# Kernel optimization log

Hardware: AMD Instinct MI355X
Metric: run time of the kernel (lower is better)

The kernel has to match this reference:

```python
import jax, jax.numpy as jnp
import numpy as np

N = 100_000      # nodes
E = 1_600_000    # edges (avg degree 16)
F_IN = 32        # node_feat_dim
HID = 32         # hidden_dim
OUT = 1          # out_dim


def setup_inputs() -> dict:
    key = jax.random.key(0)
    ks = jax.random.split(key, 16)
    x = jax.random.normal(ks[0], (N, F_IN), dtype=jnp.float32)
    # edge_index with no self loops (PyG ChebConv removes them anyway)
    src = jax.random.randint(ks[1], (E,), 0, N, dtype=jnp.int32)
    off = jax.random.randint(ks[2], (E,), 1, N, dtype=jnp.int32)
    dst = ((src + off) % N).astype(jnp.int32)
    edge_index = jnp.stack([src, dst])

    def glorot(k, shape, fan_in, fan_out):
        s = (2.0 / (fan_in + fan_out)) ** 0.5
        return (s * jax.random.normal(k, shape)).astype(jnp.float32)

    inp = {"x": x, "edge_index": edge_index}
    names = ["xz", "hz", "xr", "hr", "xh", "hh"]
    for i, nm in enumerate(names):
        fan = F_IN if nm[0] == "x" else HID
        inp[f"W_{nm}"] = glorot(ks[3 + i], (2, fan, HID), fan, HID)  # ChebConv K=2
        inp[f"b_{nm}"] = jnp.zeros((HID,), jnp.float32)
    inp["W_gcn"] = glorot(ks[9], (HID, HID), HID, HID)
    inp["b_gcn"] = jnp.zeros((HID,), jnp.float32)
    inp["W_lin"] = glorot(ks[10], (HID, OUT), HID, OUT)
    inp["b_lin"] = jnp.zeros((OUT,), jnp.float32)
    return inp


def _forward(x, edge_index, W_xz, b_xz, W_hz, b_hz, W_xr, b_xr, W_hr, b_hr,
             W_xh, b_xh, W_hh, b_hh, W_gcn, b_gcn, W_lin, b_lin):
    src, dst = edge_index[0], edge_index[1]
    ones = jnp.ones((src.shape[0],), x.dtype)

    def agg(w, v):  # out[i] = sum_{e: dst_e = i} w_e * v[src_e]
        return jax.ops.segment_sum(w[:, None] * v[src], dst, num_segments=N)

    # --- ChebConv (sym norm, lambda_max=2): L_hat = -D^{-1/2} A D^{-1/2} ---
    deg = jax.ops.segment_sum(ones, src, num_segments=N)
    dis = jnp.where(deg > 0, jax.lax.rsqrt(jnp.maximum(deg, 1.0)), 0.0)
    lap_w = -(dis[src] * dis[dst])

    def cheb(v, W, b):  # K=2: x @ W0 + (L_hat x) @ W1 + b
        return v @ W[0] + agg(lap_w, v) @ W[1] + b

    # --- GConvGRU single step, H0 = 0 ---
    H0 = jnp.zeros((N, HID), x.dtype)
    Z = jax.nn.sigmoid(cheb(x, W_xz, b_xz) + cheb(H0, W_hz, b_hz))
    R = jax.nn.sigmoid(cheb(x, W_xr, b_xr) + cheb(H0, W_hr, b_hr))
    Ht = jnp.tanh(cheb(x, W_xh, b_xh) + cheb(H0 * R, W_hh, b_hh))
    H = Z * H0 + (1.0 - Z) * Ht

    # --- GCNConv with added self loops (deg includes self loop) ---
    deg_g = jax.ops.segment_sum(ones, dst, num_segments=N) + 1.0
    disg = jax.lax.rsqrt(deg_g)
    gw = disg[src] * disg[dst]
    hw = H @ W_gcn
    h = agg(gw, hw) + (disg * disg)[:, None] * hw + b_gcn  # neighbors + self loop
    h = jax.nn.relu(h)

    out = h @ W_lin + b_lin
    return out.squeeze(-1)


def reference(x, edge_index, W_xz, b_xz, W_hz, b_hz, W_xr, b_xr, W_hr, b_hr,
              W_xh, b_xh, W_hh, b_hh, W_gcn, b_gcn, W_lin, b_lin):
    return _forward(x, edge_index, W_xz, b_xz, W_hz, b_hz, W_xr, b_xr, W_hr, b_hr,
                    W_xh, b_xh, W_hh, b_hh, W_gcn, b_gcn, W_lin, b_lin)
```

## Files before the change

kernel.cpp:

```cpp
#include <hip/hip_runtime.h>
#include <hip/hip_fp16.h>

#define NN 100000
#define NE 1600000
#define NB 391
#define NBLK 391
#define CHUNK 4096
#define BT 1024
#define PT 1024
#define ASTR 8192

__device__ __forceinline__ float h16lo(unsigned u) {
    return __half2float(__ushort_as_half((unsigned short)(u & 0xffffu)));
}
__device__ __forceinline__ float h16hi(unsigned u) {
    return __half2float(__ushort_as_half((unsigned short)(u >> 16)));
}
__device__ __forceinline__ unsigned short h16(float f) {
    return __half_as_ushort(__float2half(f));
}
__device__ __forceinline__ unsigned pack2h(float a, float b) {
    return (unsigned)h16(a) | ((unsigned)h16(b) << 16);
}

using f16x8  = __attribute__((ext_vector_type(8)))  _Float16;
using f32x16 = __attribute__((ext_vector_type(16))) float;

__global__ __launch_bounds__(BT) void k_bucket(
        const int* __restrict__ src, const int* __restrict__ dst,
        int* __restrict__ cur_d, int* __restrict__ cur_s,
        unsigned* __restrict__ bkd, unsigned char* __restrict__ bks) {
    __shared__ int hd[NB], hs[NB];
    __shared__ int bd[NB], bs[NB];
    __shared__ int od[NB], os[NB];
    __shared__ int t0[512], t1[512];
    __shared__ unsigned       sortd[CHUNK];
    __shared__ unsigned short sbkt [CHUNK];
    __shared__ unsigned char  sorts[CHUNK];
    __shared__ unsigned short sbkts[CHUNK];

    int tid = threadIdx.x, blk = blockIdx.x;
    if (tid < NB) { hd[tid] = 0; hs[tid] = 0; }
    __syncthreads();

    int e0 = blk * CHUNK, ee = min(e0 + CHUNK, NE);
    int sv[4], dv[4]; bool va[4];
#pragma unroll
    for (int u = 0; u < 4; ++u) {
        int e = e0 + u * BT + tid;
        va[u] = e < ee;
        if (va[u]) {
            sv[u] = src[e]; dv[u] = dst[e];
            atomicAdd(&hd[dv[u] >> 8], 1);
            atomicAdd(&hs[sv[u] >> 8], 1);
        }
    }
    __syncthreads();

    if (tid < 512) {
        t0[tid] = tid < NB ? hd[tid] : 0;
        t1[tid] = tid < NB ? hs[tid] : 0;
    }
    __syncthreads();
    for (int off = 1; off < 512; off <<= 1) {
        int a = 0, b = 0;
        if (tid < 512 && tid >= off) { a = t0[tid - off]; b = t1[tid - off]; }
        __syncthreads();
        if (tid < 512) { t0[tid] += a; t1[tid] += b; }
        __syncthreads();
    }
    if (tid < NB) {
        int c = hd[tid], c2 = hs[tid];
        od[tid] = t0[tid] - c;
        os[tid] = t1[tid] - c2;
        bd[tid] = c  ? atomicAdd(&cur_d[tid], c)  : 0;
        bs[tid] = c2 ? atomicAdd(&cur_s[tid], c2) : 0;
        hd[tid] = od[tid];
        hs[tid] = os[tid];
    }
    __syncthreads();

#pragma unroll
    for (int u = 0; u < 4; ++u) if (va[u]) {
        int bu = dv[u] >> 8;
        int p = atomicAdd(&hd[bu], 1);
        sortd[p] = ((unsigned)(dv[u] & 255) << 17) | (unsigned)sv[u];
        sbkt[p]  = (unsigned short)bu;
        int bv = sv[u] >> 8;
        int q = atomicAdd(&hs[bv], 1);
        sorts[q] = (unsigned char)(sv[u] & 255);
        sbkts[q] = (unsigned short)bv;
    }
    __syncthreads();

    int n = ee - e0;
    for (int i = tid; i < n; i += BT) {
        int b1 = sbkt[i];
        bkd[b1 * ASTR + bd[b1] + (i - od[b1])] = sortd[i];
        int b2 = sbkts[i];
        bks[b2 * ASTR + bs[b2] + (i - os[b2])] = sorts[i];
    }
}

__global__ __launch_bounds__(PT) void k_p2(const unsigned* __restrict__ bkd,
                                           const unsigned char* __restrict__ bks,
                                           const int* __restrict__ cur_d,
                                           const int* __restrict__ cur_s,
                                           int* __restrict__ cd,
                                           int* __restrict__ start,
                                           int* __restrict__ csr_s,
                                           float* __restrict__ dis,
                                           float* __restrict__ disg) {
    __shared__ int hist[256], scn[256], hsA[256];
    __shared__ int red[PT];
    int b = blockIdx.x, tid = threadIdx.x;
    if (tid < 256) { hist[tid] = 0; hsA[tid] = 0; }
    int acc = 0;
    for (int i = tid; i < b; i += PT) acc += cur_d[i];
    red[tid] = acc;
    __syncthreads();
    for (int off = PT / 2; off > 0; off >>= 1) {
        if (tid < off) red[tid] += red[tid + off];
        __syncthreads();
    }
    int cb = red[0];

    int eb = b * ASTR, ee = eb + cur_d[b];
    for (int e = eb + tid; e < ee; e += PT)
        atomicAdd(&hist[bkd[e] >> 17], 1);
    int sb = b * ASTR, se = sb + cur_s[b];
    for (int e = sb + tid; e < se; e += PT)
        atomicAdd(&hsA[bks[e]], 1);
    __syncthreads();
    int c = (tid < 256) ? hist[tid] : 0;
    if (tid < 256) scn[tid] = c;
    __syncthreads();
    for (int off = 1; off < 256; off <<= 1) {
        int t = (tid < 256 && tid >= off) ? scn[tid - off] : 0;
        __syncthreads();
        if (tid < 256) scn[tid] += t;
        __syncthreads();
    }
    if (tid < 256) {
        int excl = scn[tid] - c;
        int node = (b << 8) + tid;
        if (node < NN) {
            cd[node] = c;
            start[node] = cb + excl;
            int oc = hsA[tid];
            dis[node]  = oc > 0 ? rsqrtf((float)oc) : 0.0f;
            disg[node] = rsqrtf((float)c + 1.0f);
        }
    }
    __syncthreads();
    if (tid < 256) hsA[tid] = cb + scn[tid] - c;
    __syncthreads();
    for (int e = eb + tid; e < ee; e += PT) {
        unsigned pk = bkd[e];
        int p = atomicAdd(&hsA[pk >> 17], 1);
        csr_s[p] = (int)(pk & 0x1FFFFu);
    }
}

__global__ __launch_bounds__(256) void k_cvt(const float* __restrict__ x,
                                             const float* __restrict__ dis,
                                             unsigned short* __restrict__ xs,
                                             const float* __restrict__ W_xz,
                                             const float* __restrict__ W_xh,
                                             const float* __restrict__ W_gcn,
                                             unsigned short* __restrict__ BzT,
                                             unsigned short* __restrict__ BhT,
                                             unsigned short* __restrict__ WgT) {
    int tid = threadIdx.x;
    int i = blockIdx.x * 256 + tid;
    if (i < NN * 32) {
        xs[i] = h16(x[i] * dis[i >> 5]);
    } else if (blockIdx.x == (NN * 32) / 256) {
        for (int idx = tid; idx < 2048; idx += 256) {
            int f = idx >> 6, k = idx & 63;
            float vz = (k < 32) ? W_xz[k * 32 + f] : W_xz[1024 + (k - 32) * 32 + f];
            float vh = (k < 32) ? W_xh[k * 32 + f] : W_xh[1024 + (k - 32) * 32 + f];
            BzT[idx] = h16(vz);
            BhT[idx] = h16(vh);
        }
        for (int idx = tid; idx < 1024; idx += 256) {
            int f = idx >> 5, k = idx & 31;
            WgT[idx] = h16(W_gcn[k * 32 + f]);
        }
    }
}

__global__ __launch_bounds__(256) void k_gath_lx(const uint2* __restrict__ xs2,
                                                 const int* __restrict__ csr_s,
                                                 const int* __restrict__ start,
                                                 const int* __restrict__ cd,
                                                 const float* __restrict__ dis,
                                                 unsigned* __restrict__ Lxh) {
    int tid = threadIdx.x;
    int node = blockIdx.x * 8 + (tid >> 5);
    int lane = tid & 31, eoff = lane >> 3, c = lane & 7;
    int st = start[node], cn = cd[node];

    float a0 = 0.f, a1 = 0.f, a2 = 0.f, a3 = 0.f;
    for (int j = 0; j < cn; j += 8) {
        int e0 = j + eoff, e1 = j + 4 + eoff;
        int c0 = e0 < cn ? e0 : cn - 1;  float m0 = e0 < cn ? 1.0f : 0.0f;
        int c1 = e1 < cn ? e1 : cn - 1;  float m1 = e1 < cn ? 1.0f : 0.0f;
        int s0 = csr_s[st + c0], s1 = csr_s[st + c1];
        uint2 v0 = xs2[s0 * 8 + c];
        uint2 v1 = xs2[s1 * 8 + c];
        a0 = fmaf(m0, h16lo(v0.x), a0);  a1 = fmaf(m0, h16hi(v0.x), a1);
        a2 = fmaf(m0, h16lo(v0.y), a2);  a3 = fmaf(m0, h16hi(v0.y), a3);
        a0 = fmaf(m1, h16lo(v1.x), a0);  a1 = fmaf(m1, h16hi(v1.x), a1);
        a2 = fmaf(m1, h16lo(v1.y), a2);  a3 = fmaf(m1, h16hi(v1.y), a3);
    }
#pragma unroll
    for (int off = 8; off < 32; off <<= 1) {
        a0 += __shfl_xor(a0, off, 32);  a1 += __shfl_xor(a1, off, 32);
        a2 += __shfl_xor(a2, off, 32);  a3 += __shfl_xor(a3, off, 32);
    }
    if (lane < 8) {
        float w = -dis[node];
        Lxh[node * 16 + 2 * lane]     = pack2h(w * a0, w * a1);
        Lxh[node * 16 + 2 * lane + 1] = pack2h(w * a2, w * a3);
    }
}

__global__ __launch_bounds__(256) void k_dmm(
        const float* __restrict__ x,
        const f16x8* __restrict__ Lxh,
        const f16x8* __restrict__ BzT,
        const f16x8* __restrict__ BhT,
        const f16x8* __restrict__ WgT,
        const float* __restrict__ b_xz, const float* __restrict__ b_hz,
        const float* __restrict__ b_xh, const float* __restrict__ b_hh,
        const float* __restrict__ disg,
        unsigned short* __restrict__ hws) {
    __shared__ unsigned short Hl[4 * 1280];
    int tid = threadIdx.x;
    int wv = blockIdx.x * 4 + (tid >> 6);
    if (wv > 3124) wv = 3124;
    int l = tid & 63, mrow = l & 31, hi = l >> 5;
    int n0 = wv * 32;
    unsigned short* Hw = Hl + (tid >> 6) * 1280;

    f32x16 accz = {}, acct = {};
    const float* xrow = x + (size_t)(n0 + mrow) * 32;
#pragma unroll
    for (int c = 0; c < 2; ++c) {
        f16x8 a;
        const float* p = xrow + c * 16 + hi * 8;
#pragma unroll
        for (int e = 0; e < 8; ++e) a[e] = (_Float16)p[e];
        accz = __builtin_amdgcn_mfma_f32_32x32x16_f16(a, BzT[mrow * 8 + c * 2 + hi], accz, 0, 0, 0);
        acct = __builtin_amdgcn_mfma_f32_32x32x16_f16(a, BhT[mrow * 8 + c * 2 + hi], acct, 0, 0, 0);
    }
    const f16x8* Lrow = Lxh + (size_t)(n0 + mrow) * 4;
#pragma unroll
    for (int c = 2; c < 4; ++c) {
        f16x8 a = Lrow[(c - 2) * 2 + hi];
        accz = __builtin_amdgcn_mfma_f32_32x32x16_f16(a, BzT[mrow * 8 + c * 2 + hi], accz, 0, 0, 0);
        acct = __builtin_amdgcn_mfma_f32_32x32x16_f16(a, BhT[mrow * 8 + c * 2 + hi], acct, 0, 0, 0);
    }
    float bz = b_xz[mrow] + b_hz[mrow];
    float bh = b_xh[mrow] + b_hh[mrow];
#pragma unroll
    for (int j = 0; j < 16; ++j) {
        float z = accz[j] + bz, t = acct[j] + bh;
        float Z = 1.0f / (1.0f + expf(-z));
        float H = (1.0f - Z) * tanhf(t);
        int r = (j & 3) + 8 * (j >> 2) + 4 * hi;
        Hw[r * 40 + mrow] = h16(H);
    }
    f32x16 acch = {};
#pragma unroll
    for (int c = 0; c < 2; ++c) {
        f16x8 hfrag = *reinterpret_cast<const f16x8*>(&Hw[mrow * 40 + c * 16 + hi * 8]);
        acch = __builtin_amdgcn_mfma_f32_32x32x16_f16(hfrag, WgT[mrow * 4 + c * 2 + hi], acch, 0, 0, 0);
    }
#pragma unroll
    for (int j = 0; j < 16; ++j) {
        int r = (j & 3) + 8 * (j >> 2) + 4 * hi;
        int node = n0 + r;
        hws[node * 32 + mrow] = h16(disg[node] * acch[j]);
    }
}

__global__ __launch_bounds__(256) void k_gath_h(const uint2* __restrict__ hws2,
                                                const int* __restrict__ csr_s,
                                                const int* __restrict__ start,
                                                const int* __restrict__ cd,
                                                const float* __restrict__ disg,
                                                const float* __restrict__ b_gcn,
                                                const float* __restrict__ W_lin,
                                                const float* __restrict__ b_lin,
                                                float* __restrict__ out) {
    int tid = threadIdx.x;
    int node = blockIdx.x * 8 + (tid >> 5);
    int lane = tid & 31, eoff = lane >> 3, c = lane & 7;
    int st = start[node], cn = cd[node];

    float a0 = 0.f, a1 = 0.f, a2 = 0.f, a3 = 0.f;
    for (int j = 0; j < cn; j += 8) {
        int e0 = j + eoff, e1 = j + 4 + eoff;
        int c0 = e0 < cn ? e0 : cn - 1;  float m0 = e0 < cn ? 1.0f : 0.0f;
        int c1 = e1 < cn ? e1 : cn - 1;  float m1 = e1 < cn ? 1.0f : 0.0f;
        int s0 = csr_s[st + c0], s1 = csr_s[st + c1];
        uint2 v0 = hws2[s0 * 8 + c];
        uint2 v1 = hws2[s1 * 8 + c];
        a0 = fmaf(m0, h16lo(v0.x), a0);  a1 = fmaf(m0, h16hi(v0.x), a1);
        a2 = fmaf(m0, h16lo(v0.y), a2);  a3 = fmaf(m0, h16hi(v0.y), a3);
        a0 = fmaf(m1, h16lo(v1.x), a0);  a1 = fmaf(m1, h16hi(v1.x), a1);
        a2 = fmaf(m1, h16lo(v1.y), a2);  a3 = fmaf(m1, h16hi(v1.y), a3);
    }
#pragma unroll
    for (int off = 8; off < 32; off <<= 1) {
        a0 += __shfl_xor(a0, off, 32);  a1 += __shfl_xor(a1, off, 32);
        a2 += __shfl_xor(a2, off, 32);  a3 += __shfl_xor(a3, off, 32);
    }
    float p = 0.0f;
    if (lane < 8) {
        uint2 sv = hws2[node * 8 + lane];
        float dg = disg[node];
        int f0 = 4 * lane;
        float h0 = dg * (a0 + h16lo(sv.x)) + b_gcn[f0];
        float h1 = dg * (a1 + h16hi(sv.x)) + b_gcn[f0 + 1];
        float h2 = dg * (a2 + h16lo(sv.y)) + b_gcn[f0 + 2];
        float h3 = dg * (a3 + h16hi(sv.y)) + b_gcn[f0 + 3];
        p = fmaxf(h0, 0.0f) * W_lin[f0]
          + fmaxf(h1, 0.0f) * W_lin[f0 + 1]
          + fmaxf(h2, 0.0f) * W_lin[f0 + 2]
          + fmaxf(h3, 0.0f) * W_lin[f0 + 3];
    }
    p += __shfl_xor(p, 1, 32);
    p += __shfl_xor(p, 2, 32);
    p += __shfl_xor(p, 4, 32);
    if (lane == 0) out[node] = p + b_lin[0];
}

extern "C" void kernel_launch(void* const* d_in, const int* in_sizes, int n_in,
                              void* d_out, int out_size, void* d_ws, size_t ws_size,
                              hipStream_t stream) {
    const float* x     = (const float*)d_in[0];
    const int*   ei    = (const int*)d_in[1];
    const int*   src   = ei;
    const int*   dst   = ei + NE;
    const float* W_xz  = (const float*)d_in[2];
    const float* b_xz  = (const float*)d_in[3];
    const float* b_hz  = (const float*)d_in[5];
    const float* W_xh  = (const float*)d_in[10];
    const float* b_xh  = (const float*)d_in[11];
    const float* b_hh  = (const float*)d_in[13];
    const float* W_gcn = (const float*)d_in[14];
    const float* b_gcn = (const float*)d_in[15];
    const float* W_lin = (const float*)d_in[16];
    const float* b_lin = (const float*)d_in[17];
    float* out = (float*)d_out;

    int* w = (int*)d_ws;
    int* cur_d = w;                       w += 392;
    int* cur_s = w;                       w += 392;
    int* cd    = w;                       w += NN;
    int* start = w;                       w += NN;
    float* dis  = (float*)w;              w += NN;
    float* disg = (float*)w;              w += NN;
    unsigned short* hws = (unsigned short*)w;  w += 16 * NN;
    unsigned* Lxh = (unsigned*)w;         w += 16 * NN;
    unsigned* bkd = (unsigned*)w;         w += NB * ASTR;
    unsigned char* bks = (unsigned char*)w; w += (NB * ASTR) / 4;
    int* csr_s = w;                       w += NE;
    unsigned short* BzT = (unsigned short*)w; w += 1024;
    unsigned short* BhT = (unsigned short*)w; w += 1024;
    unsigned short* WgT = (unsigned short*)w; w += 512;
    unsigned short* xs = (unsigned short*)bkd;

    hipMemsetAsync(cur_d, 0, 784 * sizeof(int), stream);

    k_bucket <<<NBLK, BT, 0, stream>>>(src, dst, cur_d, cur_s, bkd, bks);
    k_p2     <<<NB, PT, 0, stream>>>(bkd, bks, cur_d, cur_s,
                                     cd, start, csr_s, dis, disg);
    k_cvt    <<<(NN * 32) / 256 + 1, 256, 0, stream>>>(x, dis, xs,
                                      W_xz, W_xh, W_gcn, BzT, BhT, WgT);
    k_gath_lx<<<NN / 8, 256, 0, stream>>>((const uint2*)xs, csr_s, start, cd,
                                          dis, Lxh);
    k_dmm    <<<782, 256, 0, stream>>>(x, (const f16x8*)Lxh, (const f16x8*)BzT,
                                       (const f16x8*)BhT, (const f16x8*)WgT,
                                       b_xz, b_hz, b_xh, b_hh, disg, hws);
    k_gath_h <<<NN / 8, 256, 0, stream>>>((const uint2*)hws, csr_s, start, cd,
                                          disg, b_gcn, W_lin, b_lin, out);
}
```

Before: 125.3 us.

## Fuse feature scaling and weight conversion into CSR build; halve bucket chunk

The separate k_cvt kernel is removed. The per-node scaling and fp16 conversion of x, plus the weight transposes, now run at the end of k_p2 using degree values the block already holds in shared memory. The xs buffer moves from aliasing bkd, which k_p2 still reads, to hws. Separately, the bucketing kernel uses 2048-edge chunks over 782 blocks to get more parallelism, at the cost of more global atomics on the bucket cursors and smaller local sorts.

```diff
diff --git a/kernel.cpp b/kernel.cpp
--- a/kernel.cpp
+++ b/kernel.cpp
@@ -4,8 +4,8 @@
 #define NN 100000
 #define NE 1600000
 #define NB 391
-#define NBLK 391
-#define CHUNK 4096
+#define NBLK 782
+#define CHUNK 2048
 #define BT 1024
 #define PT 1024
 #define ASTR 8192
@@ -44,9 +44,9 @@
     __syncthreads();
 
     int e0 = blk * CHUNK, ee = min(e0 + CHUNK, NE);
-    int sv[4], dv[4]; bool va[4];
-#pragma unroll
-    for (int u = 0; u < 4; ++u) {
+    int sv[2], dv[2]; bool va[2];
+#pragma unroll
+    for (int u = 0; u < 2; ++u) {
         int e = e0 + u * BT + tid;
         va[u] = e < ee;
         if (va[u]) {
@@ -81,7 +81,7 @@
     __syncthreads();
 
 #pragma unroll
-    for (int u = 0; u < 4; ++u) if (va[u]) {
+    for (int u = 0; u < 2; ++u) if (va[u]) {
         int bu = dv[u] >> 8;
         int p = atomicAdd(&hd[bu], 1);
         sortd[p] = ((unsigned)(dv[u] & 255) << 17) | (unsigned)sv[u];
@@ -106,12 +106,21 @@
                                            const unsigned char* __restrict__ bks,
                                            const int* __restrict__ cur_d,
                                            const int* __restrict__ cur_s,
+                                           const float* __restrict__ x,
                                            int* __restrict__ cd,
                                            int* __restrict__ start,
                                            int* __restrict__ csr_s,
                                            float* __restrict__ dis,
-                                           float* __restrict__ disg) {
+                                           float* __restrict__ disg,
+                                           unsigned short* __restrict__ xs,
+                                           const float* __restrict__ W_xz,
+                                           const float* __restrict__ W_xh,
+                                           const float* __restrict__ W_gcn,
+                                           unsigned short* __restrict__ BzT,
+                                           unsigned short* __restrict__ BhT,
+                                           unsigned short* __restrict__ WgT) {
     __shared__ int hist[256], scn[256], hsA[256];
+    __shared__ float disL[256];
     __shared__ int red[PT];
     int b = blockIdx.x, tid = threadIdx.x;
     if (tid < 256) { hist[tid] = 0; hsA[tid] = 0; }
@@ -148,7 +157,9 @@
             cd[node] = c;
             start[node] = cb + excl;
             int oc = hsA[tid];
-            dis[node]  = oc > 0 ? rsqrtf((float)oc) : 0.0f;
+            float dv = oc > 0 ? rsqrtf((float)oc) : 0.0f;
+            disL[tid]  = dv;
+            dis[node]  = dv;
             disg[node] = rsqrtf((float)c + 1.0f);
         }
     }
@@ -160,30 +171,24 @@
         int p = atomicAdd(&hsA[pk >> 17], 1);
         csr_s[p] = (int)(pk & 0x1FFFFu);
     }
-}
-
-__global__ __launch_bounds__(256) void k_cvt(const float* __restrict__ x,
-                                             const float* __restrict__ dis,
-                                             unsigned short* __restrict__ xs,
-                                             const float* __restrict__ W_xz,
-                                             const float* __restrict__ W_xh,
-                                             const float* __restrict__ W_gcn,
-                                             unsigned short* __restrict__ BzT,
-                                             unsigned short* __restrict__ BhT,
-                                             unsigned short* __restrict__ WgT) {
-    int tid = threadIdx.x;
-    int i = blockIdx.x * 256 + tid;
-    if (i < NN * 32) {
-        xs[i] = h16(x[i] * dis[i >> 5]);
-    } else if (blockIdx.x == (NN * 32) / 256) {
-        for (int idx = tid; idx < 2048; idx += 256) {
+
+    int nbase = b << 8;
+    for (int i = tid; i < 256 * 32; i += PT) {
+        int nl = i >> 5, f = i & 31;
+        int node = nbase + nl;
+        if (node < NN)
+            xs[node * 32 + f] = h16(x[node * 32 + f] * disL[nl]);
+    }
+
+    if (b == 0) {
+        for (int idx = tid; idx < 2048; idx += PT) {
             int f = idx >> 6, k = idx & 63;
             float vz = (k < 32) ? W_xz[k * 32 + f] : W_xz[1024 + (k - 32) * 32 + f];
             float vh = (k < 32) ? W_xh[k * 32 + f] : W_xh[1024 + (k - 32) * 32 + f];
             BzT[idx] = h16(vz);
             BhT[idx] = h16(vh);
         }
-        for (int idx = tid; idx < 1024; idx += 256) {
+        for (int idx = tid; idx < 1024; idx += PT) {
             int f = idx >> 5, k = idx & 31;
             WgT[idx] = h16(W_gcn[k * 32 + f]);
         }
@@ -372,15 +377,14 @@
     unsigned short* BzT = (unsigned short*)w; w += 1024;
     unsigned short* BhT = (unsigned short*)w; w += 1024;
     unsigned short* WgT = (unsigned short*)w; w += 512;
-    unsigned short* xs = (unsigned short*)bkd;
+    unsigned short* xs = hws;
 
     hipMemsetAsync(cur_d, 0, 784 * sizeof(int), stream);
 
     k_bucket <<<NBLK, BT, 0, stream>>>(src, dst, cur_d, cur_s, bkd, bks);
-    k_p2     <<<NB, PT, 0, stream>>>(bkd, bks, cur_d, cur_s,
-                                     cd, start, csr_s, dis, disg);
-    k_cvt    <<<(NN * 32) / 256 + 1, 256, 0, stream>>>(x, dis, xs,
-                                      W_xz, W_xh, W_gcn, BzT, BhT, WgT);
+    k_p2     <<<NB, PT, 0, stream>>>(bkd, bks, cur_d, cur_s, x,
+                                     cd, start, csr_s, dis, disg, xs,
+                                     W_xz, W_xh, W_gcn, BzT, BhT, WgT);
     k_gath_lx<<<NN / 8, 256, 0, stream>>>((const uint2*)xs, csr_s, start, cd,
                                           dis, Lxh);
     k_dmm    <<<782, 256, 0, stream>>>(x, (const f16x8*)Lxh, (const f16x8*)BzT,
```

After: 135.3 us. 1.08x slower.
